# Kernel tuning notes

Hardware: AMD Instinct MI355X
Metric: run time of the kernel (lower is better)

Reference implementation:

```python
import jax, jax.numpy as jnp
import numpy as np

N, E, IN, H1, H2 = 100000, 3200000, 128, 64, 64


def setup_inputs() -> dict:
    key = jax.random.key(0)
    ks = jax.random.split(key, 6)
    return {
        "edge_index": jax.random.randint(ks[0], (2, E), 0, N),
        "edge_weight": jax.random.uniform(ks[1], (E,), jnp.float32),
        "emb": jax.random.normal(ks[2], (N, IN), jnp.float32) * 0.05,  # xavier-initialized node embeddings
        "W1": jax.random.normal(ks[3], (IN, H1), jnp.float32) / np.sqrt(IN),
        "b1": jnp.zeros((H1,), jnp.float32),
        "W2": jax.random.normal(ks[4], (H1, H2), jnp.float32) / np.sqrt(H1),
        "b2": jnp.zeros((H2,), jnp.float32),
    }


def _digcn_conv(x, edge_index, edge_weight, W, b):
    # DIGCNConv: dense transform, then weighted sparse neighborhood sum-aggregation.
    x = x @ W                                              # [N, d_out]
    msg = edge_weight[:, None] * x[edge_index[0]]          # gather sources -> [E, d_out]
    out = jax.ops.segment_sum(msg, edge_index[1], num_segments=x.shape[0])  # scatter-add to targets
    return out + b


def reference(edge_index, edge_weight, emb, W1, b1, W2, b2):
    h = jax.nn.relu(_digcn_conv(emb, edge_index, edge_weight, W1, b1))
    # F.dropout with training=False is identity (inference mode)
    return _digcn_conv(h, edge_index, edge_weight, W2, b2)
```

## Files before the change

### kernel.cpp

```cpp
#include <hip/hip_runtime.h>
#include <hip/hip_bf16.h>

#define NNODES 100000
#define DIN 128
#define DH 64
#define SRCMASK 0x1FFFF
#define BSH2 8
#define BN2 256
#define NBUCK2 ((NNODES + BN2 - 1) >> BSH2)
#define NCAP 8448
#define EPB 8192
#define MAXBLK 512

typedef short s16x8 __attribute__((ext_vector_type(8)));
typedef float f32x4 __attribute__((ext_vector_type(4)));

static __device__ __forceinline__ short f2bf(float f) {
  __hip_bfloat16 h = __float2bfloat16(f);
  return *reinterpret_cast<short*>(&h);
}
static __device__ __forceinline__ float bf2f(short s) {
  return __uint_as_float(((unsigned)(unsigned short)s) << 16);
}


__global__ __launch_bounds__(256, 4) void gemm1_mfma(
    const float* __restrict__ emb, const float* __restrict__ W1,
    __hip_bfloat16* __restrict__ x1, int N) {
  __shared__ short Bhi[4 * 4 * 64 * 8];
  __shared__ short Blo[4 * 4 * 64 * 8];
  int tid = threadIdx.x;

  for (int idx = tid; idx < 8192; idx += 256) {
    int i = idx & 7, ln = (idx >> 3) & 63, ct = (idx >> 9) & 3, kc = idx >> 11;
    int k = kc * 32 + (ln >> 4) * 8 + i;
    int col = ct * 16 + (ln & 15);
    float w = W1[k * DH + col];
    short h = f2bf(w);
    Bhi[idx] = h;
    Blo[idx] = f2bf(w - bf2f(h));
  }
  __syncthreads();

  int lane = tid & 63, wv = tid >> 6;
  int r0 = (blockIdx.x * 8 + wv * 2) * 16;
  if (r0 >= N) return;

  const int rA = lane & 15, g = lane >> 4;
  f32x4 acc[2][4] = {};

#pragma unroll
  for (int kc = 0; kc < 4; ++kc) {
    s16x8 ahi[2], alo[2];
#pragma unroll
    for (int rt = 0; rt < 2; ++rt) {
      int r = r0 + rt * 16 + rA;
      float av[8];
      if (r < N) {
        const float4* ap = (const float4*)(emb + (long)r * DIN + kc * 32 + g * 8);
        float4 v0 = ap[0], v1 = ap[1];
        av[0] = v0.x; av[1] = v0.y; av[2] = v0.z; av[3] = v0.w;
        av[4] = v1.x; av[5] = v1.y; av[6] = v1.z; av[7] = v1.w;
      } else {
#pragma unroll
        for (int i = 0; i < 8; ++i) av[i] = 0.f;
      }
#pragma unroll
      for (int i = 0; i < 8; ++i) {
        short h = f2bf(av[i]);
        ahi[rt][i] = h;
        alo[rt][i] = f2bf(av[i] - bf2f(h));
      }
    }
#pragma unroll
    for (int ct = 0; ct < 4; ++ct) {
      int fo = ((kc * 4 + ct) * 64 + lane) * 8;
      s16x8 bh = *(const s16x8*)&Bhi[fo];
      s16x8 bl = *(const s16x8*)&Blo[fo];
#pragma unroll
      for (int rt = 0; rt < 2; ++rt) {
        acc[rt][ct] = __builtin_amdgcn_mfma_f32_16x16x32_bf16(ahi[rt], bh, acc[rt][ct], 0, 0, 0);
        acc[rt][ct] = __builtin_amdgcn_mfma_f32_16x16x32_bf16(alo[rt], bh, acc[rt][ct], 0, 0, 0);
        acc[rt][ct] = __builtin_amdgcn_mfma_f32_16x16x32_bf16(ahi[rt], bl, acc[rt][ct], 0, 0, 0);
      }
    }
  }

#pragma unroll
  for (int rt = 0; rt < 2; ++rt) {
#pragma unroll
    for (int j = 0; j < 4; ++j) {
      int row = r0 + rt * 16 + g * 4 + j;
      if (row < N) {
#pragma unroll
        for (int ct = 0; ct < 4; ++ct)
          x1[(long)row * DH + ct * 16 + rA] = __float2bfloat16(acc[rt][ct][j]);
      }
    }
  }
}

__global__ __launch_bounds__(256, 4) void gemm2_mfma(
    const float* __restrict__ agg, const float* __restrict__ W2,
    const float* __restrict__ b1, __hip_bfloat16* __restrict__ x2, int N) {
  __shared__ short Bhi[2 * 4 * 64 * 8];
  __shared__ short Blo[2 * 4 * 64 * 8];
  int tid = threadIdx.x;

  for (int idx = tid; idx < 4096; idx += 256) {
    int i = idx & 7, ln = (idx >> 3) & 63, ct = (idx >> 9) & 3, kc = (idx >> 11) & 1;
    int k = kc * 32 + (ln >> 4) * 8 + i;
    int col = ct * 16 + (ln & 15);
    float w = W2[k * DH + col];
    short h = f2bf(w);
    Bhi[idx] = h;
    Blo[idx] = f2bf(w - bf2f(h));
  }
  __syncthreads();

  int lane = tid & 63, wv = tid >> 6;
  int r0 = (blockIdx.x * 8 + wv * 2) * 16;
  if (r0 >= N) return;

  const int rA = lane & 15, g = lane >> 4;
  f32x4 acc[2][4] = {};

#pragma unroll
  for (int kc = 0; kc < 2; ++kc) {
    const float4* bp = (const float4*)(b1 + kc * 32 + g * 8);
    float4 b0 = bp[0], b4 = bp[1];
    float bv[8] = {b0.x, b0.y, b0.z, b0.w, b4.x, b4.y, b4.z, b4.w};
    s16x8 ahi[2], alo[2];
#pragma unroll
    for (int rt = 0; rt < 2; ++rt) {
      int r = r0 + rt * 16 + rA;
      float av[8];
      if (r < N) {
        const float4* ap = (const float4*)(agg + (long)r * DH + kc * 32 + g * 8);
        float4 v0 = ap[0], v1 = ap[1];
        av[0] = v0.x; av[1] = v0.y; av[2] = v0.z; av[3] = v0.w;
        av[4] = v1.x; av[5] = v1.y; av[6] = v1.z; av[7] = v1.w;
      } else {
#pragma unroll
        for (int i = 0; i < 8; ++i) av[i] = -1e30f;
      }
#pragma unroll
      for (int i = 0; i < 8; ++i) {
        float a = fmaxf(av[i] + bv[i], 0.f);
        short h = f2bf(a);
        ahi[rt][i] = h;
        alo[rt][i] = f2bf(a - bf2f(h));
      }
    }
#pragma unroll
    for (int ct = 0; ct < 4; ++ct) {
      int fo = ((kc * 4 + ct) * 64 + lane) * 8;
      s16x8 bh = *(const s16x8*)&Bhi[fo];
      s16x8 bl = *(const s16x8*)&Blo[fo];
#pragma unroll
      for (int rt = 0; rt < 2; ++rt) {
        acc[rt][ct] = __builtin_amdgcn_mfma_f32_16x16x32_bf16(ahi[rt], bh, acc[rt][ct], 0, 0, 0);
        acc[rt][ct] = __builtin_amdgcn_mfma_f32_16x16x32_bf16(alo[rt], bh, acc[rt][ct], 0, 0, 0);
        acc[rt][ct] = __builtin_amdgcn_mfma_f32_16x16x32_bf16(ahi[rt], bl, acc[rt][ct], 0, 0, 0);
      }
    }
  }

#pragma unroll
  for (int rt = 0; rt < 2; ++rt) {
#pragma unroll
    for (int j = 0; j < 4; ++j) {
      int row = r0 + rt * 16 + g * 4 + j;
      if (row < N) {
#pragma unroll
        for (int ct = 0; ct < 4; ++ct)
          x2[(long)row * DH + ct * 16 + rA] = __float2bfloat16(acc[rt][ct][j]);
      }
    }
  }
}


__global__ __launch_bounds__(512, 6) void block_sort(
    const int* __restrict__ srcs, const int* __restrict__ dsts,
    const float* __restrict__ w, int* __restrict__ spk,
    unsigned char* __restrict__ sdl, unsigned short* __restrict__ offTab,
    int* __restrict__ bTot, int E) {
  __shared__ int stageP[EPB];
  __shared__ unsigned char stageD[EPB];
  __shared__ int hist[512];
  __shared__ int sc[512];
  __shared__ int cur[512];
  int tid = threadIdx.x, blk = blockIdx.x;
  int e0 = blk * EPB;

  hist[tid] = 0;
  __syncthreads();

  int pk[16], bd[16];
#pragma unroll
  for (int i = 0; i < 16; ++i) {
    int e = e0 + i * 512 + tid;
    if (e < E) {
      int s = srcs[e], d = dsts[e];
      float wv = w[e];
      int q = (int)(wv * 32768.f + 0.5f);
      if (q > 32767) q = 32767;
      pk[i] = (s & SRCMASK) | (q << 17);
      bd[i] = d;
    } else bd[i] = -1;
  }
#pragma unroll
  for (int i = 0; i < 16; ++i)
    if (bd[i] >= 0) atomicAdd(&hist[bd[i] >> BSH2], 1);
  __syncthreads();

  if (tid < NBUCK2 && hist[tid]) atomicAdd(&bTot[tid], hist[tid]);

  sc[tid] = (tid < NBUCK2) ? hist[tid] : 0;
  __syncthreads();
  for (int d = 1; d < 512; d <<= 1) {
    int u = (tid >= d) ? sc[tid - d] : 0;
    __syncthreads();
    sc[tid] += u;
    __syncthreads();
  }
  long row = (long)blk * (NBUCK2 + 1);
  if (tid < NBUCK2) {
    int base = sc[tid] - hist[tid];
    cur[tid] = base;
    offTab[row + tid] = (unsigned short)base;
    if (tid == NBUCK2 - 1) offTab[row + NBUCK2] = (unsigned short)sc[tid];
  }
  __syncthreads();

#pragma unroll
  for (int i = 0; i < 16; ++i) {
    if (bd[i] >= 0) {
      int pos = atomicAdd(&cur[bd[i] >> BSH2], 1);
      stageP[pos] = pk[i];
      stageD[pos] = (unsigned char)(bd[i] & (BN2 - 1));
    }
  }
  __syncthreads();

  int eN = min(EPB, E - e0);
  for (int i = tid; i < eN; i += 512) {
    spk[(long)blk * EPB + i] = stageP[i];
    sdl[(long)blk * EPB + i] = stageD[i];
  }
}

__global__ __launch_bounds__(512, 6) void gather_gemm1(
    const unsigned short* __restrict__ offTab, const int* __restrict__ spk,
    const unsigned char* __restrict__ sdl, const int* __restrict__ bTot,
    int* __restrict__ noff, int* __restrict__ ndeg, int* __restrict__ pairs,
    int NBLK, int N,
    const float* __restrict__ emb, const float* __restrict__ W1,
    __hip_bfloat16* __restrict__ x1, int NB2) {
  __shared__ __align__(16) char smem[50432];
  __shared__ int shb;
  int tid = threadIdx.x;

  if ((int)blockIdx.x >= NB2) {
    short* Bhi = (short*)smem;
    short* Blo = Bhi + 8192;
    for (int idx = tid; idx < 8192; idx += 512) {
      int i = idx & 7, ln = (idx >> 3) & 63, ct = (idx >> 9) & 3, kc = idx >> 11;
      int k = kc * 32 + (ln >> 4) * 8 + i;
      int col = ct * 16 + (ln & 15);
      float wv = W1[k * DH + col];
      short h = f2bf(wv);
      Bhi[idx] = h;
      Blo[idx] = f2bf(wv - bf2f(h));
    }
    __syncthreads();

    int lane = tid & 63, wv8 = tid >> 6;
    int gblk = blockIdx.x - NB2;
    int r0 = gblk * 256 + wv8 * 32;
    if (r0 >= N) return;

    const int rA = lane & 15, g = lane >> 4;
    f32x4 acc[2][4] = {};

#pragma unroll
    for (int kc = 0; kc < 4; ++kc) {
      s16x8 ahi[2], alo[2];
#pragma unroll
      for (int rt = 0; rt < 2; ++rt) {
        int r = r0 + rt * 16 + rA;
        float av[8];
        if (r < N) {
          const float4* ap = (const float4*)(emb + (long)r * DIN + kc * 32 + g * 8);
          float4 v0 = ap[0], v1 = ap[1];
          av[0] = v0.x; av[1] = v0.y; av[2] = v0.z; av[3] = v0.w;
          av[4] = v1.x; av[5] = v1.y; av[6] = v1.z; av[7] = v1.w;
        } else {
#pragma unroll
          for (int i = 0; i < 8; ++i) av[i] = 0.f;
        }
#pragma unroll
        for (int i = 0; i < 8; ++i) {
          short h = f2bf(av[i]);
          ahi[rt][i] = h;
          alo[rt][i] = f2bf(av[i] - bf2f(h));
        }
      }
#pragma unroll
      for (int ct = 0; ct < 4; ++ct) {
        int fo = ((kc * 4 + ct) * 64 + lane) * 8;
        s16x8 bh = *(const s16x8*)&Bhi[fo];
        s16x8 bl = *(const s16x8*)&Blo[fo];
#pragma unroll
        for (int rt = 0; rt < 2; ++rt) {
          acc[rt][ct] = __builtin_amdgcn_mfma_f32_16x16x32_bf16(ahi[rt], bh, acc[rt][ct], 0, 0, 0);
          acc[rt][ct] = __builtin_amdgcn_mfma_f32_16x16x32_bf16(alo[rt], bh, acc[rt][ct], 0, 0, 0);
          acc[rt][ct] = __builtin_amdgcn_mfma_f32_16x16x32_bf16(ahi[rt], bl, acc[rt][ct], 0, 0, 0);
        }
      }
    }

#pragma unroll
    for (int rt = 0; rt < 2; ++rt) {
#pragma unroll
      for (int j = 0; j < 4; ++j) {
        int row = r0 + rt * 16 + g * 4 + j;
        if (row < N) {
#pragma unroll
          for (int ct = 0; ct < 4; ++ct)
            x1[(long)row * DH + ct * 16 + rA] = __float2bfloat16(acc[rt][ct][j]);
        }
      }
    }
    return;
  }

  int b = blockIdx.x;
  int* gathP = (int*)smem;
  unsigned char* gathD = (unsigned char*)(smem + NCAP * 4);
  unsigned short* offR = (unsigned short*)(smem + NCAP * 5);
  unsigned short* cntR = offR + MAXBLK;
  int* baseR = (int*)(smem + NCAP * 5 + MAXBLK * 4);
  int* sc = baseR + MAXBLK;
  int* deg = sc + 512;
  int* cur = deg + BN2;

  sc[tid] = (tid < NBUCK2) ? bTot[tid] : 0;
  __syncthreads();
  for (int d = 1; d < 512; d <<= 1) {
    int u = (tid >= d) ? sc[tid - d] : 0;
    __syncthreads();
    sc[tid] += u;
    __syncthreads();
  }
  if (tid == 0) shb = (b == 0) ? 0 : sc[b - 1];
  __syncthreads();
  int bstart = shb;

  for (int blk = tid; blk < NBLK; blk += 512) {
    long row = (long)blk * (NBUCK2 + 1);
    int st = offTab[row + b];
    int en = offTab[row + b + 1];
    offR[blk] = (unsigned short)st;
    cntR[blk] = (unsigned short)(en - st);
  }
  __syncthreads();
  sc[tid] = (tid < NBLK) ? (int)cntR[tid] : 0;
  __syncthreads();
  for (int d = 1; d < 512; d <<= 1) {
    int u = (tid >= d) ? sc[tid - d] : 0;
    __syncthreads();
    sc[tid] += u;
    __syncthreads();
  }
  if (tid < NBLK) baseR[tid] = sc[tid] - (int)cntR[tid];
  if (tid < BN2) deg[tid] = 0;
  __syncthreads();
  int total = sc[NBLK - 1];

  if (total <= NCAP) {
    for (int g = tid; g < total; g += 512) {
      int lo = 0, hi = NBLK - 1;
      while (lo < hi) {
        int mid = (lo + hi + 1) >> 1;
        if (baseR[mid] <= g) lo = mid; else hi = mid - 1;
      }
      int pos = (int)offR[lo] + (g - baseR[lo]);
      gathP[g] = spk[(long)lo * EPB + pos];
      gathD[g] = sdl[(long)lo * EPB + pos];
    }
    __syncthreads();
    for (int k = tid; k < total; k += 512)
      atomicAdd(&deg[gathD[k]], 1);
    __syncthreads();
    sc[tid] = (tid < BN2) ? deg[tid] : 0;
    __syncthreads();
    for (int d = 1; d < 512; d <<= 1) {
      int u = (tid >= d) ? sc[tid - d] : 0;
      __syncthreads();
      sc[tid] += u;
      __syncthreads();
    }
    if (tid < BN2) {
      int excl = sc[tid] - deg[tid];
      cur[tid] = bstart + excl;
      int n = (b << BSH2) + tid;
      if (n < N) { noff[n] = bstart + excl; ndeg[n] = deg[tid]; }
    }
    __syncthreads();
    for (int k = tid; k < total; k += 512) {
      int p = atomicAdd(&cur[gathD[k]], 1);
      pairs[p] = gathP[k];
    }
  } else {
    for (int g = tid; g < total; g += 512) {
      int lo = 0, hi = NBLK - 1;
      while (lo < hi) {
        int mid = (lo + hi + 1) >> 1;
        if (baseR[mid] <= g) lo = mid; else hi = mid - 1;
      }
      int pos = (int)offR[lo] + (g - baseR[lo]);
      atomicAdd(&deg[sdl[(long)lo * EPB + pos]], 1);
    }
    __syncthreads();
    sc[tid] = (tid < BN2) ? deg[tid] : 0;
    __syncthreads();
    for (int d = 1; d < 512; d <<= 1) {
      int u = (tid >= d) ? sc[tid - d] : 0;
      __syncthreads();
      sc[tid] += u;
      __syncthreads();
    }
    if (tid < BN2) {
      int excl = sc[tid] - deg[tid];
      cur[tid] = bstart + excl;
      int n = (b << BSH2) + tid;
      if (n < N) { noff[n] = bstart + excl; ndeg[n] = deg[tid]; }
    }
    __syncthreads();
    for (int g = tid; g < total; g += 512) {
      int lo = 0, hi = NBLK - 1;
      while (lo < hi) {
        int mid = (lo + hi + 1) >> 1;
        if (baseR[mid] <= g) lo = mid; else hi = mid - 1;
      }
      int pos = (int)offR[lo] + (g - baseR[lo]);
      int pk = spk[(long)lo * EPB + pos];
      int dl = sdl[(long)lo * EPB + pos];
      int p = atomicAdd(&cur[dl], 1);
      pairs[p] = pk;
    }
  }
}

#define ACC4(P, XV)                                          \
  do {                                                       \
    float wv_ = (float)((P) >> 17) * (1.f / 32768.f);        \
    a0 += wv_ * __uint_as_float((XV).x << 16);               \
    a1 += wv_ * __uint_as_float((XV).x & 0xFFFF0000u);       \
    a2 += wv_ * __uint_as_float((XV).y << 16);               \
    a3 += wv_ * __uint_as_float((XV).y & 0xFFFF0000u);       \
  } while (0)

__global__ __launch_bounds__(256) void agg_quad(
    const int* __restrict__ pairs, const int* __restrict__ noff,
    const int* __restrict__ ndeg,
    const uint2* __restrict__ x,
    const float* __restrict__ bias, float* __restrict__ out, int N) {
  int wid = (int)(((long)blockIdx.x * 256 + threadIdx.x) >> 6);
  int lane = threadIdx.x & 63;
  if (wid >= N) return;
  int h = lane >> 4;
  int fj = lane & 15;
  int st = noff[wid];
  int m = ndeg[wid];
  float a0 = 0.f, a1 = 0.f, a2 = 0.f, a3 = 0.f;

  for (int base = 0; base < m; base += 64) {
    int pl = (base + lane < m) ? pairs[st + base + lane] : 0;
    int mm = m - base;

    unsigned pg[8];
#pragma unroll
    for (int g = 0; g < 8; ++g) pg[g] = (unsigned)__shfl(pl, g * 4 + h);
    uint2 xg[8];
#pragma unroll
    for (int g = 0; g < 8; ++g) xg[g] = x[(pg[g] & SRCMASK) * 16 + fj];
#pragma unroll
    for (int g = 0; g < 8; ++g) ACC4(pg[g], xg[g]);

#pragma unroll
    for (int q = 32; q < 64; q += 16) {
      if (q >= mm) break;
      unsigned p0 = (unsigned)__shfl(pl, q + h);
      unsigned p1 = (unsigned)__shfl(pl, q + 4 + h);
      unsigned p2 = (unsigned)__shfl(pl, q + 8 + h);
      unsigned p3 = (unsigned)__shfl(pl, q + 12 + h);
      uint2 y0 = x[(p0 & SRCMASK) * 16 + fj];
      uint2 y1 = x[(p1 & SRCMASK) * 16 + fj];
      uint2 y2 = x[(p2 & SRCMASK) * 16 + fj];
      uint2 y3 = x[(p3 & SRCMASK) * 16 + fj];
      ACC4(p0, y0); ACC4(p1, y1); ACC4(p2, y2); ACC4(p3, y3);
    }
  }

  a0 += __shfl_xor(a0, 16); a0 += __shfl_xor(a0, 32);
  a1 += __shfl_xor(a1, 16); a1 += __shfl_xor(a1, 32);
  a2 += __shfl_xor(a2, 16); a2 += __shfl_xor(a2, 32);
  a3 += __shfl_xor(a3, 16); a3 += __shfl_xor(a3, 32);
  if (lane < 16) {
    if (bias) {
      float4 bv = ((const float4*)bias)[fj];
      a0 += bv.x; a1 += bv.y; a2 += bv.z; a3 += bv.w;
    }
    ((float4*)out)[(long)wid * 16 + fj] = make_float4(a0, a1, a2, a3);
  }
}


__global__ __launch_bounds__(256) void gemm1_f32(
    const float* __restrict__ emb, const float* __restrict__ W1,
    float* __restrict__ x1, int N) {
  __shared__ float Ws[DIN * DH];
  __shared__ float rows[4][DIN];
  int tid = threadIdx.x;
  for (int i = tid; i < DIN * DH; i += 256) Ws[i] = W1[i];
  int r0 = blockIdx.x * 4;
  for (int i = tid; i < 4 * DIN; i += 256) {
    int rr = i >> 7, kk = i & 127;
    int r = r0 + rr;
    rows[rr][kk] = (r < N) ? emb[(long)r * DIN + kk] : 0.f;
  }
  __syncthreads();
  int rr = tid >> 6, j = tid & 63;
  int r = r0 + rr;
  float acc = 0.f;
#pragma unroll
  for (int k = 0; k < DIN; ++k) acc += rows[rr][k] * Ws[k * DH + j];
  if (r < N) x1[(long)r * DH + j] = acc;
}

__global__ __launch_bounds__(256) void gemm2_f32(
    const float* __restrict__ agg, const float* __restrict__ W2,
    const float* __restrict__ b1, float* __restrict__ x2, int N) {
  __shared__ float Ws[DH * DH];
  __shared__ float rows[4][DH];
  int tid = threadIdx.x;
  for (int i = tid; i < DH * DH; i += 256) Ws[i] = W2[i];
  int r0 = blockIdx.x * 4;
  {
    int rr = tid >> 6, kk = tid & 63;
    int r = r0 + rr;
    float v = (r < N) ? agg[(long)r * DH + kk] + b1[kk] : 0.f;
    rows[rr][kk] = v > 0.f ? v : 0.f;
  }
  __syncthreads();
  int rr = tid >> 6, j = tid & 63;
  float acc = 0.f;
#pragma unroll
  for (int k = 0; k < DH; ++k) acc += rows[rr][k] * Ws[k * DH + j];
  int r = r0 + rr;
  if (r < N) x2[(long)r * DH + j] = acc;
}

__global__ __launch_bounds__(256) void init_bias_kernel(
    float* __restrict__ out, const float* __restrict__ b2, int total) {
  int i = blockIdx.x * 256 + threadIdx.x;
  if (i < total) out[i] = b2[i & 63];
}

__global__ __launch_bounds__(256) void scatter_kernel(
    const int* __restrict__ srcs, const int* __restrict__ dsts,
    const float* __restrict__ w, const float* __restrict__ x,
    float* __restrict__ out, int E) {
  long t = (long)blockIdx.x * 256 + threadIdx.x;
  long e = t >> 6;
  if (e >= E) return;
  int j = (int)(t & 63);
  int s = srcs[e];
  int d = dsts[e];
  float val = w[e] * x[(long)s * DH + j];
  atomicAdd(&out[(long)d * DH + j], val);
}


static inline size_t align256(size_t x) { return (x + 255) & ~(size_t)255; }

extern "C" void kernel_launch(void* const* d_in, const int* in_sizes, int n_in,
                              void* d_out, int out_size, void* d_ws, size_t ws_size,
                              hipStream_t stream) {
  const int*   edge_index = (const int*)d_in[0];
  const float* edge_w     = (const float*)d_in[1];
  const float* emb        = (const float*)d_in[2];
  const float* W1         = (const float*)d_in[3];
  const float* b1         = (const float*)d_in[4];
  const float* W2         = (const float*)d_in[5];
  const float* b2         = (const float*)d_in[6];
  float* out = (float*)d_out;

  const int E = in_sizes[0] / 2;
  const int N = NNODES;
  const int* srcs = edge_index;
  const int* dsts = edge_index + E;

  const int NBLK = (E + EPB - 1) / EPB;

  const size_t spkbytes    = (size_t)NBLK * EPB * sizeof(int);
  const size_t sdlbytes    = (size_t)NBLK * EPB;
  const size_t xbytes_bf   = (size_t)N * DH * sizeof(__hip_bfloat16);
  const size_t offTabbytes = (size_t)NBLK * (NBUCK2 + 1) * sizeof(unsigned short);
  const size_t pairsbytes  = (size_t)E * sizeof(int);
  const size_t nbytes      = (size_t)N * sizeof(int);

  const int aggBlocks = (N + 3) / 4;
  const int gemmBlocks = (N + 127) / 128;
  const int g1Blocks   = (N + 255) / 256;

  size_t off = 0;
  char* base = (char*)d_ws;
  int* spk = (int*)(base + off);                   off = align256(off + spkbytes);
  unsigned char* sdl = (unsigned char*)(base + off); off = align256(off + sdlbytes);
  __hip_bfloat16* xbuf = (__hip_bfloat16*)(base + off); off = align256(off + xbytes_bf);
  unsigned short* offTab = (unsigned short*)(base + off); off = align256(off + offTabbytes);
  int* pairs = (int*)(base + off);  off = align256(off + pairsbytes);
  int* noff  = (int*)(base + off);  off = align256(off + nbytes);
  int* ndeg  = (int*)(base + off);  off = align256(off + nbytes);
  int* bTot  = (int*)(base + off);  off = align256(off + NBUCK2 * sizeof(int));
  const size_t needed_fused = off;

  if (ws_size >= needed_fused && NBLK <= MAXBLK) {
    hipMemsetAsync(bTot, 0, NBUCK2 * sizeof(int), stream);
    block_sort<<<NBLK, 512, 0, stream>>>(srcs, dsts, edge_w, spk, sdl, offTab, bTot, E);
    gather_gemm1<<<NBUCK2 + g1Blocks, 512, 0, stream>>>(
        offTab, spk, sdl, bTot, noff, ndeg, pairs, NBLK, N, emb, W1, xbuf, NBUCK2);
    agg_quad<<<aggBlocks, 256, 0, stream>>>(pairs, noff, ndeg, (const uint2*)xbuf,
                                            nullptr, out, N);
    gemm2_mfma<<<gemmBlocks, 256, 0, stream>>>(out, W2, b1, xbuf, N);
    agg_quad<<<aggBlocks, 256, 0, stream>>>(pairs, noff, ndeg, (const uint2*)xbuf,
                                            b2, out, N);
    return;
  }

  off = 0;
  int* spk2 = (int*)(base + off);
  off = align256(off + (spkbytes > xbytes_bf ? spkbytes : xbytes_bf));
  __hip_bfloat16* xbuf2 = (__hip_bfloat16*)spk2;
  unsigned char* sdl2 = (unsigned char*)(base + off); off = align256(off + sdlbytes);
  unsigned short* offTab2 = (unsigned short*)(base + off); off = align256(off + offTabbytes);
  int* pairs2 = (int*)(base + off);  off = align256(off + pairsbytes);
  int* noff2  = (int*)(base + off);  off = align256(off + nbytes);
  int* ndeg2  = (int*)(base + off);  off = align256(off + nbytes);
  int* bTot2  = (int*)(base + off);  off = align256(off + NBUCK2 * sizeof(int));
  const size_t needed_seq = off;

  if (ws_size >= needed_seq && NBLK <= MAXBLK) {
    hipMemsetAsync(bTot2, 0, NBUCK2 * sizeof(int), stream);
    block_sort<<<NBLK, 512, 0, stream>>>(srcs, dsts, edge_w, spk2, sdl2, offTab2, bTot2, E);
    gather_gemm1<<<NBUCK2, 512, 0, stream>>>(
        offTab2, spk2, sdl2, bTot2, noff2, ndeg2, pairs2, NBLK, N, emb, W1, xbuf2, NBUCK2);
    gemm1_mfma<<<gemmBlocks, 256, 0, stream>>>(emb, W1, xbuf2, N);
    agg_quad<<<aggBlocks, 256, 0, stream>>>(pairs2, noff2, ndeg2, (const uint2*)xbuf2,
                                            nullptr, out, N);
    gemm2_mfma<<<gemmBlocks, 256, 0, stream>>>(out, W2, b1, xbuf2, N);
    agg_quad<<<aggBlocks, 256, 0, stream>>>(pairs2, noff2, ndeg2, (const uint2*)xbuf2,
                                            b2, out, N);
    return;
  }

  const long scatterThreads = (long)E * 64;
  const int scatterBlocks = (int)((scatterThreads + 255) / 256);
  const int rowBlocks4 = (N + 3) / 4;
  float* xb1 = (float*)d_ws;

  gemm1_f32<<<rowBlocks4, 256, 0, stream>>>(emb, W1, xb1, N);
  hipMemsetAsync(d_out, 0, (size_t)N * DH * sizeof(float), stream);
  scatter_kernel<<<scatterBlocks, 256, 0, stream>>>(srcs, dsts, edge_w, xb1, out, E);

  gemm2_f32<<<rowBlocks4, 256, 0, stream>>>(out, W2, b1, xb1, N);
  init_bias_kernel<<<(N * DH + 255) / 256, 256, 0, stream>>>(out, b2, N * DH);
  scatter_kernel<<<scatterBlocks, 256, 0, stream>>>(srcs, dsts, edge_w, xb1, out, E);
}
```

Baseline: 186.6 us.

## Replace LDS edge staging with per-thread contiguous ranges and cursor walk

The counting-sort bucket pass no longer stages each bucket's edges in shared memory. Each thread now takes a contiguous range of edges, finds its start with one binary search, and walks forward with a cursor, reading the global spk/sdl arrays twice (once for the degree count, once for the scatter). This removes the per-element binary search and shrinks the LDS footprint from about 50KB to 32KB, which could allow more resident blocks, including for the GEMM blocks that share this kernel. The cost is a second global read of the edge data and uncoalesced per-thread strided accesses.

```diff
diff --git a/kernel.cpp b/kernel.cpp
--- a/kernel.cpp
+++ b/kernel.cpp
@@ -8,7 +8,6 @@
 #define BSH2 8
 #define BN2 256
 #define NBUCK2 ((NNODES + BN2 - 1) >> BSH2)
-#define NCAP 8448
 #define EPB 8192
 #define MAXBLK 512
 
@@ -258,7 +257,7 @@
     int NBLK, int N,
     const float* __restrict__ emb, const float* __restrict__ W1,
     __hip_bfloat16* __restrict__ x1, int NB2) {
-  __shared__ __align__(16) char smem[50432];
+  __shared__ __align__(16) char smem[32768];
   __shared__ int shb;
   int tid = threadIdx.x;
 
@@ -337,14 +336,12 @@
   }
 
   int b = blockIdx.x;
-  int* gathP = (int*)smem;
-  unsigned char* gathD = (unsigned char*)(smem + NCAP * 4);
-  unsigned short* offR = (unsigned short*)(smem + NCAP * 5);
+  unsigned short* offR = (unsigned short*)smem;
   unsigned short* cntR = offR + MAXBLK;
-  int* baseR = (int*)(smem + NCAP * 5 + MAXBLK * 4);
-  int* sc = baseR + MAXBLK;
-  int* deg = sc + 512;
-  int* cur = deg + BN2;
+  int* baseR = (int*)(smem + 2048);
+  int* sc    = baseR + MAXBLK;
+  int* deg   = sc + 512;
+  int* cur   = deg + BN2;
 
   sc[tid] = (tid < NBUCK2) ? bTot[tid] : 0;
   __syncthreads();
@@ -379,77 +376,52 @@
   __syncthreads();
   int total = sc[NBLK - 1];
 
-  if (total <= NCAP) {
-    for (int g = tid; g < total; g += 512) {
-      int lo = 0, hi = NBLK - 1;
-      while (lo < hi) {
-        int mid = (lo + hi + 1) >> 1;
-        if (baseR[mid] <= g) lo = mid; else hi = mid - 1;
-      }
-      int pos = (int)offR[lo] + (g - baseR[lo]);
-      gathP[g] = spk[(long)lo * EPB + pos];
-      gathD[g] = sdl[(long)lo * EPB + pos];
-    }
-    __syncthreads();
-    for (int k = tid; k < total; k += 512)
-      atomicAdd(&deg[gathD[k]], 1);
-    __syncthreads();
-    sc[tid] = (tid < BN2) ? deg[tid] : 0;
-    __syncthreads();
-    for (int d = 1; d < 512; d <<= 1) {
-      int u = (tid >= d) ? sc[tid - d] : 0;
-      __syncthreads();
-      sc[tid] += u;
-      __syncthreads();
-    }
-    if (tid < BN2) {
-      int excl = sc[tid] - deg[tid];
-      cur[tid] = bstart + excl;
-      int n = (b << BSH2) + tid;
-      if (n < N) { noff[n] = bstart + excl; ndeg[n] = deg[tid]; }
-    }
-    __syncthreads();
-    for (int k = tid; k < total; k += 512) {
-      int p = atomicAdd(&cur[gathD[k]], 1);
-      pairs[p] = gathP[k];
-    }
-  } else {
-    for (int g = tid; g < total; g += 512) {
-      int lo = 0, hi = NBLK - 1;
-      while (lo < hi) {
-        int mid = (lo + hi + 1) >> 1;
-        if (baseR[mid] <= g) lo = mid; else hi = mid - 1;
-      }
-      int pos = (int)offR[lo] + (g - baseR[lo]);
-      atomicAdd(&deg[sdl[(long)lo * EPB + pos]], 1);
-    }
-    __syncthreads();
-    sc[tid] = (tid < BN2) ? deg[tid] : 0;
-    __syncthreads();
-    for (int d = 1; d < 512; d <<= 1) {
-      int u = (tid >= d) ? sc[tid - d] : 0;
-      __syncthreads();
-      sc[tid] += u;
-      __syncthreads();
-    }
-    if (tid < BN2) {
-      int excl = sc[tid] - deg[tid];
-      cur[tid] = bstart + excl;
-      int n = (b << BSH2) + tid;
-      if (n < N) { noff[n] = bstart + excl; ndeg[n] = deg[tid]; }
-    }
-    __syncthreads();
-    for (int g = tid; g < total; g += 512) {
-      int lo = 0, hi = NBLK - 1;
-      while (lo < hi) {
-        int mid = (lo + hi + 1) >> 1;
-        if (baseR[mid] <= g) lo = mid; else hi = mid - 1;
-      }
-      int pos = (int)offR[lo] + (g - baseR[lo]);
-      int pk = spk[(long)lo * EPB + pos];
-      int dl = sdl[(long)lo * EPB + pos];
+  int per = (total + 511) >> 9;
+  int gbeg = tid * per;
+  int gend = min(total, gbeg + per);
+  int lo = 0, cbase = 0, cend = 0, coff = 0;
+  if (gbeg < gend) {
+    int l = 0, h2 = NBLK - 1;
+    while (l < h2) {
+      int mid = (l + h2 + 1) >> 1;
+      if (baseR[mid] <= gbeg) l = mid; else h2 = mid - 1;
+    }
+    lo = l; cbase = baseR[lo]; cend = cbase + (int)cntR[lo]; coff = (int)offR[lo];
+  }
+
+  {
+    int l2 = lo, cb = cbase, ce = cend, co = coff;
+    for (int g = gbeg; g < gend; ++g) {
+      while (g >= ce) { ++l2; cb = baseR[l2]; ce = cb + (int)cntR[l2]; co = (int)offR[l2]; }
+      atomicAdd(&deg[sdl[(long)l2 * EPB + co + (g - cb)]], 1);
+    }
+  }
+  __syncthreads();
+
+  sc[tid] = (tid < BN2) ? deg[tid] : 0;
+  __syncthreads();
+  for (int d = 1; d < 512; d <<= 1) {
+    int u = (tid >= d) ? sc[tid - d] : 0;
+    __syncthreads();
+    sc[tid] += u;
+    __syncthreads();
+  }
+  if (tid < BN2) {
+    int excl = sc[tid] - deg[tid];
+    cur[tid] = bstart + excl;
+    int n = (b << BSH2) + tid;
+    if (n < N) { noff[n] = bstart + excl; ndeg[n] = deg[tid]; }
+  }
+  __syncthreads();
+
+  {
+    int l2 = lo, cb = cbase, ce = cend, co = coff;
+    for (int g = gbeg; g < gend; ++g) {
+      while (g >= ce) { ++l2; cb = baseR[l2]; ce = cb + (int)cntR[l2]; co = (int)offR[l2]; }
+      long src = (long)l2 * EPB + co + (g - cb);
+      int dl = sdl[src];
       int p = atomicAdd(&cur[dl], 1);
-      pairs[p] = pk;
+      pairs[p] = spk[src];
     }
   }
 }
```

After: 259.9 us. 39.2% more time.
